# Kernel tuning notes

Hardware: AMD Instinct MI355X
Metric: run time of the kernel (lower is better)

Reference implementation:

```python
import jax, jax.numpy as jnp
import numpy as np

D_MODEL = 1024
NUM_HEADS = 16
HEAD_DIM = D_MODEL // NUM_HEADS
ROPE_THETA = 10000.0


def apply_rope(x, positions):
    # x: (B, H, S, Dh), positions: (S,) int
    half = x.shape[-1] // 2
    inv_freq = ROPE_THETA ** (-jnp.arange(half, dtype=jnp.float32) * 2.0 / x.shape[-1])  # (Dh/2,)
    ang = positions.astype(jnp.float32)[:, None] * inv_freq[None, :]  # (S, Dh/2)
    cos, sin = jnp.cos(ang), jnp.sin(ang)
    x1 = x[..., 0::2]  # (B,H,S,Dh/2)
    x2 = x[..., 1::2]
    r1 = x1 * cos - x2 * sin
    r2 = x1 * sin + x2 * cos
    return jnp.stack([r1, r2], axis=-1).reshape(x.shape)


def setup_inputs() -> dict:
    key = jax.random.key(0)
    ks = jax.random.split(key, 5)
    B, S = 2, 2048
    scale = 1.0 / np.sqrt(D_MODEL)
    x = jax.random.normal(ks[0], (B, S, D_MODEL), dtype=jnp.float32)
    Wq = jax.random.normal(ks[1], (D_MODEL, D_MODEL), dtype=jnp.float32) * scale
    Wk = jax.random.normal(ks[2], (D_MODEL, D_MODEL), dtype=jnp.float32) * scale
    Wv = jax.random.normal(ks[3], (D_MODEL, D_MODEL), dtype=jnp.float32) * scale
    Wo = jax.random.normal(ks[4], (D_MODEL, D_MODEL), dtype=jnp.float32) * scale
    token_positions = jnp.arange(S, dtype=jnp.int32)
    return {"x": x, "token_positions": token_positions, "Wq": Wq, "Wk": Wk, "Wv": Wv, "Wo": Wo}


def reference(x, token_positions, Wq, Wk, Wv, Wo):
    B, S, _ = x.shape
    # Linear is bias-free: y = x @ W.T (W: [out, in])
    def proj(W):
        y = jnp.einsum('bsd,ed->bse', x, W)
        return y.reshape(B, S, NUM_HEADS, HEAD_DIM).transpose(0, 2, 1, 3)  # (B,H,S,Dh)
    q, k, v = proj(Wq), proj(Wk), proj(Wv)
    q = apply_rope(q, token_positions)
    k = apply_rope(k, token_positions)
    scores = jnp.einsum('bhqd,bhkd->bhqk', q, k) / jnp.sqrt(jnp.float32(HEAD_DIM))
    causal = jnp.tril(jnp.ones((S, S), dtype=bool))
    scores = jnp.where(causal, scores, -jnp.inf)
    attn = jax.nn.softmax(scores, axis=-1)
    out = jnp.einsum('bhqk,bhkd->bhqd', attn, v)  # (B,H,S,Dh)
    out = out.transpose(0, 2, 1, 3).reshape(B, S, D_MODEL)
    return jnp.einsum('bsd,ed->bse', out, Wo)
```

## Files before the change

kernel.cpp:

```cpp
#include <hip/hip_runtime.h>


typedef unsigned short u16;
typedef unsigned int   u32;
typedef unsigned long long u64;
using s16x8 = __attribute__((ext_vector_type(8))) short;
using f32x4 = __attribute__((ext_vector_type(4))) float;

__device__ __forceinline__ u16 f2bf(float f) {
  union { float f; u32 u; } v; v.f = f;
  return (u16)((v.u + 0x7fffu + ((v.u >> 16) & 1u)) >> 16);
}
__device__ __forceinline__ float bf2f(u16 h) {
  union { u32 u; float f; } v; v.u = ((u32)h) << 16;
  return v.f;
}

__device__ __forceinline__ void gl2lds(const u16* g, u16* l) {
  __builtin_amdgcn_global_load_lds(
      (const __attribute__((address_space(1))) void*)g,
      (__attribute__((address_space(3))) void*)l, 16, 0, 0);
}

__global__ __launch_bounds__(256) void cvt_all(
    const float* __restrict__ x,
    const float* __restrict__ wq, const float* __restrict__ wk,
    const float* __restrict__ wv, const float* __restrict__ wo,
    u16* __restrict__ xb, u16* __restrict__ wqb, u16* __restrict__ wkb,
    u16* __restrict__ wvb, u16* __restrict__ wob) {
  int e = (blockIdx.x * 256 + threadIdx.x) * 4;
  const float* src; u16* dst; int off;
  const int XN = 4 << 20;
  if (e < XN) { src = x; dst = xb; off = e; }
  else {
    int t = e - XN; int sel = t >> 20; off = t & ((1 << 20) - 1);
    src = sel == 0 ? wq : sel == 1 ? wk : sel == 2 ? wv : wo;
    dst = sel == 0 ? wqb : sel == 1 ? wkb : sel == 2 ? wvb : wob;
  }
  float4 v = *(const float4*)(src + off);
  ushort4 o;
  o.x = f2bf(v.x); o.y = f2bf(v.y); o.z = f2bf(v.z); o.w = f2bf(v.w);
  *(ushort4*)(dst + off) = o;
}

__device__ __forceinline__ void gemm_core(
    const u16* __restrict__ A, const u16* __restrict__ W,
    u16* As, u16* Bs, int bm0, int bn0, f32x4 (&acc)[4][4]) {
  const int K = 1024;
  int tid = threadIdx.x;
  int wid = tid >> 6, lane = tid & 63, quad = lane >> 4, l15 = lane & 15;
  int wm = (wid >> 1) * 64, wn = (wid & 1) * 64;
  int ch0 = wid * 128 + lane, ch1 = ch0 + 64;
  int r0 = ch0 >> 2, c0 = (ch0 & 3) * 8;
  int r1 = ch1 >> 2, c1 = (ch1 & 3) * 8;
  const u16* Ab = A + (size_t)bm0 * K;
  const u16* Wb = W + (size_t)bn0 * K;
  u16* lA0 = As + wid * 1024; u16* lA1 = lA0 + 512;
  u16* lB0 = Bs + wid * 1024; u16* lB1 = lB0 + 512;
  for (int k0 = 0; k0 < K; k0 += 32) {
    __syncthreads();
    gl2lds(Ab + (size_t)r0 * K + k0 + c0, lA0);
    gl2lds(Ab + (size_t)r1 * K + k0 + c1, lA1);
    gl2lds(Wb + (size_t)r0 * K + k0 + c0, lB0);
    gl2lds(Wb + (size_t)r1 * K + k0 + c1, lB1);
    __syncthreads();
    s16x8 af[4], bf[4];
#pragma unroll
    for (int mi = 0; mi < 4; mi++)
      af[mi] = *(const s16x8*)(As + (wm + mi * 16 + l15) * 32 + quad * 8);
#pragma unroll
    for (int ni = 0; ni < 4; ni++)
      bf[ni] = *(const s16x8*)(Bs + (wn + ni * 16 + l15) * 32 + quad * 8);
#pragma unroll
    for (int mi = 0; mi < 4; mi++)
#pragma unroll
      for (int ni = 0; ni < 4; ni++)
        acc[mi][ni] = __builtin_amdgcn_mfma_f32_16x16x32_bf16(
            af[mi], bf[ni], acc[mi][ni], 0, 0, 0);
  }
}

__global__ __launch_bounds__(256) void gemm_qkv(
    const u16* __restrict__ xb,
    const u16* __restrict__ wq, const u16* __restrict__ wk,
    const u16* __restrict__ wv,
    u16* __restrict__ qh, u16* __restrict__ kh, u16* __restrict__ vt) {
  __shared__ __align__(16) u16 As[128 * 32];
  __shared__ __align__(16) u16 Bs[128 * 32];
  int z = blockIdx.z;
  const u16* W = (z == 0) ? wq : (z == 1) ? wk : wv;
  int bm0 = blockIdx.y * 128, bn0 = blockIdx.x * 128;
  f32x4 acc[4][4];
  const f32x4 fz = {0.f, 0.f, 0.f, 0.f};
#pragma unroll
  for (int mi = 0; mi < 4; mi++)
#pragma unroll
    for (int ni = 0; ni < 4; ni++) acc[mi][ni] = fz;
  gemm_core(xb, W, As, Bs, bm0, bn0, acc);
  int tid = threadIdx.x, wid = tid >> 6, lane = tid & 63;
  int quad = lane >> 4, l15 = lane & 15;
  int wm = (wid >> 1) * 64, wn = (wid & 1) * 64;
  if (z < 2) {
    u16* dst = (z == 0) ? qh : kh;
#pragma unroll
    for (int mi = 0; mi < 4; mi++)
#pragma unroll
      for (int ni = 0; ni < 4; ni++)
#pragma unroll
        for (int r = 0; r < 4; r++) {
          int row = bm0 + wm + mi * 16 + quad * 4 + r;
          int col = bn0 + wn + ni * 16 + l15;
          int b = row >> 11, s = row & 2047, h = col >> 6, d = col & 63;
          dst[(((size_t)(b * 16 + h)) * 2048 + s) * 64 + d] =
              f2bf(acc[mi][ni][r]);
        }
  } else {
#pragma unroll
    for (int mi = 0; mi < 4; mi++)
#pragma unroll
      for (int ni = 0; ni < 4; ni++) {
        int row0 = bm0 + wm + mi * 16 + quad * 4;
        int col = bn0 + wn + ni * 16 + l15;
        int b = row0 >> 11, s0 = row0 & 2047, h = col >> 6, d = col & 63;
        u64 pk = (u64)f2bf(acc[mi][ni][0]) |
                 ((u64)f2bf(acc[mi][ni][1]) << 16) |
                 ((u64)f2bf(acc[mi][ni][2]) << 32) |
                 ((u64)f2bf(acc[mi][ni][3]) << 48);
        *(u64*)(vt + (((size_t)(b * 16 + h)) * 64 + d) * 2048 + s0) = pk;
      }
  }
}

__global__ __launch_bounds__(256) void gemm_out(
    const u16* __restrict__ ao, const u16* __restrict__ wo,
    float* __restrict__ out) {
  __shared__ __align__(16) u16 As[128 * 32];
  __shared__ __align__(16) u16 Bs[128 * 32];
  int bm0 = blockIdx.y * 128, bn0 = blockIdx.x * 128;
  f32x4 acc[4][4];
  const f32x4 fz = {0.f, 0.f, 0.f, 0.f};
#pragma unroll
  for (int mi = 0; mi < 4; mi++)
#pragma unroll
    for (int ni = 0; ni < 4; ni++) acc[mi][ni] = fz;
  gemm_core(ao, wo, As, Bs, bm0, bn0, acc);
  int tid = threadIdx.x, wid = tid >> 6, lane = tid & 63;
  int quad = lane >> 4, l15 = lane & 15;
  int wm = (wid >> 1) * 64, wn = (wid & 1) * 64;
#pragma unroll
  for (int mi = 0; mi < 4; mi++)
#pragma unroll
    for (int ni = 0; ni < 4; ni++)
#pragma unroll
      for (int r = 0; r < 4; r++) {
        int row = bm0 + wm + mi * 16 + quad * 4 + r;
        int col = bn0 + wn + ni * 16 + l15;
        out[(size_t)row * 1024 + col] = acc[mi][ni][r];
      }
}

__global__ __launch_bounds__(256) void rope_k(
    u16* __restrict__ qh, u16* __restrict__ kh, const int* __restrict__ pos) {
  int i = blockIdx.x * 256 + threadIdx.x;
  int pair = i & 31;
  int s = (i >> 5) & 2047;
  int hb = i >> 16;
  float p = (float)pos[s];
  float freq = __expf(-0.28782313662425572f * (float)pair);
  float ang = p * freq, sn, cs;
  sincosf(ang, &sn, &cs);
  size_t base = ((size_t)hb * 2048 + s) * 64 + 2 * pair;
  {
    u32 u = *(const u32*)(qh + base);
    float x1 = bf2f((u16)(u & 0xffff)), x2 = bf2f((u16)(u >> 16));
    float r1 = (x1 * cs - x2 * sn) * 0.125f;
    float r2 = (x1 * sn + x2 * cs) * 0.125f;
    *(u32*)(qh + base) = (u32)f2bf(r1) | ((u32)f2bf(r2) << 16);
  }
  {
    u32 u = *(const u32*)(kh + base);
    float x1 = bf2f((u16)(u & 0xffff)), x2 = bf2f((u16)(u >> 16));
    float r1 = x1 * cs - x2 * sn;
    float r2 = x1 * sn + x2 * cs;
    *(u32*)(kh + base) = (u32)f2bf(r1) | ((u32)f2bf(r2) << 16);
  }
}

#define KTS 72
#define VTS 72
#define PTS 40
#define OTS 72

__global__ __launch_bounds__(256, 4) void attn_k(
    const u16* __restrict__ qh, const u16* __restrict__ kh,
    const u16* __restrict__ vt, u16* __restrict__ ao) {
  __shared__ __align__(16) u16 ks[64 * KTS];
  __shared__ __align__(16) u16 vs[64 * VTS];
  __shared__ __align__(16) u16 pt[4 * 16 * PTS];
  int bid = blockIdx.x;
  int bh = bid & 31, pi = bid >> 5;
  int b = bh >> 4, h = bh & 15;
  int tid = threadIdx.x, wid = tid >> 6, lane = tid & 63;
  int quad = lane >> 4, l15 = lane & 15;
  int qsub = wid & 1, thalf = wid >> 1;
  const u16* qbase = qh + (size_t)bh * 2048 * 64;
  const u16* kbase = kh + (size_t)bh * 2048 * 64;
  const u16* vbase = vt + (size_t)bh * 64 * 2048;
  u16* ptw = pt + wid * 16 * PTS;
  const f32x4 fz = {0.f, 0.f, 0.f, 0.f};
  int srow = tid >> 2, sc = (tid & 3) * 8;

#pragma unroll
  for (int phase = 0; phase < 2; phase++) {
    int qt = phase ? (63 - pi) : pi;
    int q0 = qt * 32, q0w = q0 + qsub * 16;
    s16x8 qf0 = *(const s16x8*)(qbase + (size_t)(q0w + l15) * 64 + quad * 8);
    s16x8 qf1 = *(const s16x8*)(qbase + (size_t)(q0w + l15) * 64 + 32 + quad * 8);
    f32x4 acc[4];
#pragma unroll
    for (int md = 0; md < 4; md++) acc[md] = fz;
    float lsum = 0.f;
    int qg = q0w + l15;
    int nt = (qt >> 1) + 1;
    uint4 rk0 = *(const uint4*)(kbase + (size_t)srow * 64 + sc);
    uint4 rk1 = *(const uint4*)(kbase + (size_t)srow * 64 + sc + 32);
    uint4 rv0 = *(const uint4*)(vbase + (size_t)srow * 2048 + sc);
    uint4 rv1 = *(const uint4*)(vbase + (size_t)srow * 2048 + sc + 32);
    for (int it = 0; it < nt; it++) {
      __syncthreads();
      *(uint4*)(ks + srow * KTS + sc) = rk0;
      *(uint4*)(ks + srow * KTS + sc + 32) = rk1;
      *(uint4*)(vs + srow * VTS + sc) = rv0;
      *(uint4*)(vs + srow * VTS + sc + 32) = rv1;
      if (it + 1 < nt) {
        int t1 = (it + 1) << 6;
        rk0 = *(const uint4*)(kbase + (size_t)(t1 + srow) * 64 + sc);
        rk1 = *(const uint4*)(kbase + (size_t)(t1 + srow) * 64 + sc + 32);
        rv0 = *(const uint4*)(vbase + (size_t)srow * 2048 + t1 + sc);
        rv1 = *(const uint4*)(vbase + (size_t)srow * 2048 + t1 + sc + 32);
      }
      __syncthreads();
      int t0 = it << 6, tb = thalf * 32;
      bool diag = (it == nt - 1);
#pragma unroll
      for (int mt = 0; mt < 2; mt++) {
        int krow = tb + mt * 16 + l15;
        s16x8 ka0 = *(const s16x8*)(ks + krow * KTS + quad * 8);
        s16x8 ka1 = *(const s16x8*)(ks + krow * KTS + 32 + quad * 8);
        f32x4 st = __builtin_amdgcn_mfma_f32_16x16x32_bf16(ka0, qf0, fz, 0, 0, 0);
        st = __builtin_amdgcn_mfma_f32_16x16x32_bf16(ka1, qf1, st, 0, 0, 0);
        u64 pk = 0;
#pragma unroll
        for (int r = 0; r < 4; r++) {
          float p = __expf(st[r]);
          if (diag) {
            int tg = t0 + tb + mt * 16 + quad * 4 + r;
            if (tg > qg) p = 0.f;
          }
          lsum += p;
          pk |= ((u64)f2bf(p)) << (16 * r);
        }
        *(u64*)(ptw + l15 * PTS + mt * 16 + quad * 4) = pk;
      }
      s16x8 pb = *(const s16x8*)(ptw + l15 * PTS + quad * 8);
#pragma unroll
      for (int md = 0; md < 4; md++) {
        s16x8 va = *(const s16x8*)(vs + (md * 16 + l15) * VTS + tb + quad * 8);
        acc[md] = __builtin_amdgcn_mfma_f32_16x16x32_bf16(va, pb, acc[md], 0, 0, 0);
      }
    }
    lsum += __shfl_xor(lsum, 16, 64);
    lsum += __shfl_xor(lsum, 32, 64);
    __syncthreads();
    float* redo = (float*)ks;
    float* redl = (float*)vs;
    if (thalf == 1) {
#pragma unroll
      for (int md = 0; md < 4; md++)
#pragma unroll
        for (int r = 0; r < 4; r++)
          redo[(qsub * 64 + lane) * 16 + md * 4 + r] = acc[md][r];
      redl[qsub * 64 + lane] = lsum;
    }
    __syncthreads();
    if (thalf == 0) {
#pragma unroll
      for (int md = 0; md < 4; md++)
#pragma unroll
        for (int r = 0; r < 4; r++)
          acc[md][r] += redo[(qsub * 64 + lane) * 16 + md * 4 + r];
      lsum += redl[qsub * 64 + lane];
      float rl = 1.0f / lsum;
      u16* ow = pt + qsub * 16 * OTS;
#pragma unroll
      for (int md = 0; md < 4; md++) {
        u64 ok = 0;
#pragma unroll
        for (int r = 0; r < 4; r++)
          ok |= ((u64)f2bf(acc[md][r] * rl)) << (16 * r);
        *(u64*)(ow + l15 * OTS + md * 16 + quad * 4) = ok;
      }
      int qq = lane >> 2, dc = lane & 3;
      uint4 o0 = *(uint4*)(ow + qq * OTS + dc * 16);
      uint4 o1 = *(uint4*)(ow + qq * OTS + dc * 16 + 8);
      size_t orow = (size_t)b * 2048 + q0 + qsub * 16 + qq;
      *(uint4*)(ao + orow * 1024 + h * 64 + dc * 16) = o0;
      *(uint4*)(ao + orow * 1024 + h * 64 + dc * 16 + 8) = o1;
    }
  }
}

extern "C" void kernel_launch(void* const* d_in, const int* in_sizes, int n_in,
                              void* d_out, int out_size, void* d_ws,
                              size_t ws_size, hipStream_t stream) {
  const float* x  = (const float*)d_in[0];
  const int* pos  = (const int*)d_in[1];
  const float* Wq = (const float*)d_in[2];
  const float* Wk = (const float*)d_in[3];
  const float* Wv = (const float*)d_in[4];
  const float* Wo = (const float*)d_in[5];
  float* out = (float*)d_out;

  char* ws = (char*)d_ws;
  const size_t MB = 1u << 20;
  u16* xb  = (u16*)(ws);
  u16* wqb = (u16*)(ws + 8 * MB);
  u16* wkb = (u16*)(ws + 10 * MB);
  u16* wvb = (u16*)(ws + 12 * MB);
  u16* wob = (u16*)(ws + 14 * MB);
  u16* qhb = (u16*)(ws + 16 * MB);
  u16* khb = (u16*)(ws + 24 * MB);
  u16* vtb = (u16*)(ws + 32 * MB);
  u16* ao  = xb;

  cvt_all<<<8192, 256, 0, stream>>>(x, Wq, Wk, Wv, Wo,
                                    xb, wqb, wkb, wvb, wob);
  gemm_qkv<<<dim3(8, 32, 3), 256, 0, stream>>>(xb, wqb, wkb, wvb,
                                               qhb, khb, vtb);
  rope_k<<<8192, 256, 0, stream>>>(qhb, khb, pos);
  attn_k<<<1024, 256, 0, stream>>>(qhb, khb, vtb, ao);
  gemm_out<<<dim3(8, 32), 256, 0, stream>>>(ao, wob, out);
}
```

Measured before the change: 214.8 us.

## Fuse RoPE into QKV GEMM epilogue and load K/V fragments directly in attention

Applies rotary embedding (and the softmax scale folded with log2e) inside the QKV GEMM epilogue using a lane shuffle to fetch the pair partner, eliminating the separate rope kernel and its extra read/write of Q and K. The attention kernel stops staging K/V tiles in LDS and instead loads MFMA fragments directly from global memory with register prefetch, removing per-tile barriers; exp is switched to exp2. The trade-off is less coalesced global loads and more sincos work per GEMM output element.

Measured after the change: 493.0 us. +129.5%, slower.

```diff
diff --git a/kernel.cpp b/kernel.cpp
--- a/kernel.cpp
+++ b/kernel.cpp
@@ -10,10 +10,6 @@
 __device__ __forceinline__ u16 f2bf(float f) {
   union { float f; u32 u; } v; v.f = f;
   return (u16)((v.u + 0x7fffu + ((v.u >> 16) & 1u)) >> 16);
-}
-__device__ __forceinline__ float bf2f(u16 h) {
-  union { u32 u; float f; } v; v.u = ((u32)h) << 16;
-  return v.f;
 }
 
 __device__ __forceinline__ void gl2lds(const u16* g, u16* l) {
@@ -83,7 +79,7 @@
 __global__ __launch_bounds__(256) void gemm_qkv(
     const u16* __restrict__ xb,
     const u16* __restrict__ wq, const u16* __restrict__ wk,
-    const u16* __restrict__ wv,
+    const u16* __restrict__ wv, const int* __restrict__ pos,
     u16* __restrict__ qh, u16* __restrict__ kh, u16* __restrict__ vt) {
   __shared__ __align__(16) u16 As[128 * 32];
   __shared__ __align__(16) u16 Bs[128 * 32];
@@ -102,18 +98,33 @@
   int wm = (wid >> 1) * 64, wn = (wid & 1) * 64;
   if (z < 2) {
     u16* dst = (z == 0) ? qh : kh;
+    float sc = (z == 0) ? 0.18033688011112042f : 1.0f;
+    float frq[4], sgn[4];
+#pragma unroll
+    for (int ni = 0; ni < 4; ni++) {
+      int d = (bn0 + wn + ni * 16 + l15) & 63;
+      frq[ni] = __expf(-0.28782313662425572f * (float)(d >> 1));
+      sgn[ni] = (d & 1) ? 1.f : -1.f;
+    }
 #pragma unroll
     for (int mi = 0; mi < 4; mi++)
 #pragma unroll
-      for (int ni = 0; ni < 4; ni++)
-#pragma unroll
-        for (int r = 0; r < 4; r++) {
-          int row = bm0 + wm + mi * 16 + quad * 4 + r;
+      for (int r = 0; r < 4; r++) {
+        int row = bm0 + wm + mi * 16 + quad * 4 + r;
+        int b = row >> 11, s = row & 2047;
+        float pv = (float)pos[s];
+#pragma unroll
+        for (int ni = 0; ni < 4; ni++) {
+          float v = acc[mi][ni][r];
+          float prt = __shfl_xor(v, 1, 64);
+          float ang = pv * frq[ni], sn, cs;
+          sincosf(ang, &sn, &cs);
+          float res = (v * cs + sgn[ni] * prt * sn) * sc;
           int col = bn0 + wn + ni * 16 + l15;
-          int b = row >> 11, s = row & 2047, h = col >> 6, d = col & 63;
-          dst[(((size_t)(b * 16 + h)) * 2048 + s) * 64 + d] =
-              f2bf(acc[mi][ni][r]);
+          int h = col >> 6, d = col & 63;
+          dst[(((size_t)(b * 16 + h)) * 2048 + s) * 64 + d] = f2bf(res);
         }
+      }
   } else {
 #pragma unroll
     for (int mi = 0; mi < 4; mi++)
@@ -159,44 +170,15 @@
       }
 }
 
-__global__ __launch_bounds__(256) void rope_k(
-    u16* __restrict__ qh, u16* __restrict__ kh, const int* __restrict__ pos) {
-  int i = blockIdx.x * 256 + threadIdx.x;
-  int pair = i & 31;
-  int s = (i >> 5) & 2047;
-  int hb = i >> 16;
-  float p = (float)pos[s];
-  float freq = __expf(-0.28782313662425572f * (float)pair);
-  float ang = p * freq, sn, cs;
-  sincosf(ang, &sn, &cs);
-  size_t base = ((size_t)hb * 2048 + s) * 64 + 2 * pair;
-  {
-    u32 u = *(const u32*)(qh + base);
-    float x1 = bf2f((u16)(u & 0xffff)), x2 = bf2f((u16)(u >> 16));
-    float r1 = (x1 * cs - x2 * sn) * 0.125f;
-    float r2 = (x1 * sn + x2 * cs) * 0.125f;
-    *(u32*)(qh + base) = (u32)f2bf(r1) | ((u32)f2bf(r2) << 16);
-  }
-  {
-    u32 u = *(const u32*)(kh + base);
-    float x1 = bf2f((u16)(u & 0xffff)), x2 = bf2f((u16)(u >> 16));
-    float r1 = x1 * cs - x2 * sn;
-    float r2 = x1 * sn + x2 * cs;
-    *(u32*)(kh + base) = (u32)f2bf(r1) | ((u32)f2bf(r2) << 16);
-  }
-}
-
-#define KTS 72
-#define VTS 72
 #define PTS 40
 #define OTS 72
 
 __global__ __launch_bounds__(256, 4) void attn_k(
     const u16* __restrict__ qh, const u16* __restrict__ kh,
     const u16* __restrict__ vt, u16* __restrict__ ao) {
-  __shared__ __align__(16) u16 ks[64 * KTS];
-  __shared__ __align__(16) u16 vs[64 * VTS];
   __shared__ __align__(16) u16 pt[4 * 16 * PTS];
+  __shared__ float redo[128 * 17];
+  __shared__ float redl[128];
   int bid = blockIdx.x;
   int bh = bid & 31, pi = bid >> 5;
   int b = bh >> 4, h = bh & 15;
@@ -208,10 +190,11 @@
   const u16* vbase = vt + (size_t)bh * 64 * 2048;
   u16* ptw = pt + wid * 16 * PTS;
   const f32x4 fz = {0.f, 0.f, 0.f, 0.f};
-  int srow = tid >> 2, sc = (tid & 3) * 8;
+  int tb = thalf * 32;
 
 #pragma unroll
   for (int phase = 0; phase < 2; phase++) {
+    __syncthreads();
     int qt = phase ? (63 - pi) : pi;
     int q0 = qt * 32, q0w = q0 + qsub * 16;
     s16x8 qf0 = *(const s16x8*)(qbase + (size_t)(q0w + l15) * 64 + quad * 8);
@@ -222,37 +205,38 @@
     float lsum = 0.f;
     int qg = q0w + l15;
     int nt = (qt >> 1) + 1;
-    uint4 rk0 = *(const uint4*)(kbase + (size_t)srow * 64 + sc);
-    uint4 rk1 = *(const uint4*)(kbase + (size_t)srow * 64 + sc + 32);
-    uint4 rv0 = *(const uint4*)(vbase + (size_t)srow * 2048 + sc);
-    uint4 rv1 = *(const uint4*)(vbase + (size_t)srow * 2048 + sc + 32);
+    s16x8 ka[4];
+    {
+      const u16* kr = kbase + (size_t)(tb + l15) * 64 + quad * 8;
+      ka[0] = *(const s16x8*)(kr);
+      ka[1] = *(const s16x8*)(kr + 32);
+      ka[2] = *(const s16x8*)(kr + 1024);
+      ka[3] = *(const s16x8*)(kr + 1024 + 32);
+    }
     for (int it = 0; it < nt; it++) {
-      __syncthreads();
-      *(uint4*)(ks + srow * KTS + sc) = rk0;
-      *(uint4*)(ks + srow * KTS + sc + 32) = rk1;
-      *(uint4*)(vs + srow * VTS + sc) = rv0;
-      *(uint4*)(vs + srow * VTS + sc + 32) = rv1;
+      int t0 = it << 6;
+      s16x8 va[4];
+#pragma unroll
+      for (int md = 0; md < 4; md++)
+        va[md] = *(const s16x8*)(vbase + (size_t)(md * 16 + l15) * 2048 +
+                                 t0 + tb + quad * 8);
+      s16x8 kn[4];
       if (it + 1 < nt) {
-        int t1 = (it + 1) << 6;
-        rk0 = *(const uint4*)(kbase + (size_t)(t1 + srow) * 64 + sc);
-        rk1 = *(const uint4*)(kbase + (size_t)(t1 + srow) * 64 + sc + 32);
-        rv0 = *(const uint4*)(vbase + (size_t)srow * 2048 + t1 + sc);
-        rv1 = *(const uint4*)(vbase + (size_t)srow * 2048 + t1 + sc + 32);
-      }
-      __syncthreads();
-      int t0 = it << 6, tb = thalf * 32;
+        const u16* kr = kbase + (size_t)(t0 + 64 + tb + l15) * 64 + quad * 8;
+        kn[0] = *(const s16x8*)(kr);
+        kn[1] = *(const s16x8*)(kr + 32);
+        kn[2] = *(const s16x8*)(kr + 1024);
+        kn[3] = *(const s16x8*)(kr + 1024 + 32);
+      }
       bool diag = (it == nt - 1);
 #pragma unroll
       for (int mt = 0; mt < 2; mt++) {
-        int krow = tb + mt * 16 + l15;
-        s16x8 ka0 = *(const s16x8*)(ks + krow * KTS + quad * 8);
-        s16x8 ka1 = *(const s16x8*)(ks + krow * KTS + 32 + quad * 8);
-        f32x4 st = __builtin_amdgcn_mfma_f32_16x16x32_bf16(ka0, qf0, fz, 0, 0, 0);
-        st = __builtin_amdgcn_mfma_f32_16x16x32_bf16(ka1, qf1, st, 0, 0, 0);
+        f32x4 st = __builtin_amdgcn_mfma_f32_16x16x32_bf16(ka[2 * mt], qf0, fz, 0, 0, 0);
+        st = __builtin_amdgcn_mfma_f32_16x16x32_bf16(ka[2 * mt + 1], qf1, st, 0, 0, 0);
         u64 pk = 0;
 #pragma unroll
         for (int r = 0; r < 4; r++) {
-          float p = __expf(st[r]);
+          float p = __builtin_amdgcn_exp2f(st[r]);
           if (diag) {
             int tg = t0 + tb + mt * 16 + quad * 4 + r;
             if (tg > qg) p = 0.f;
@@ -264,22 +248,19 @@
       }
       s16x8 pb = *(const s16x8*)(ptw + l15 * PTS + quad * 8);
 #pragma unroll
-      for (int md = 0; md < 4; md++) {
-        s16x8 va = *(const s16x8*)(vs + (md * 16 + l15) * VTS + tb + quad * 8);
-        acc[md] = __builtin_amdgcn_mfma_f32_16x16x32_bf16(va, pb, acc[md], 0, 0, 0);
-      }
+      for (int md = 0; md < 4; md++)
+        acc[md] = __builtin_amdgcn_mfma_f32_16x16x32_bf16(va[md], pb, acc[md], 0, 0, 0);
+#pragma unroll
+      for (int j = 0; j < 4; j++) ka[j] = kn[j];
     }
     lsum += __shfl_xor(lsum, 16, 64);
     lsum += __shfl_xor(lsum, 32, 64);
-    __syncthreads();
-    float* redo = (float*)ks;
-    float* redl = (float*)vs;
     if (thalf == 1) {
 #pragma unroll
       for (int md = 0; md < 4; md++)
 #pragma unroll
         for (int r = 0; r < 4; r++)
-          redo[(qsub * 64 + lane) * 16 + md * 4 + r] = acc[md][r];
+          redo[(qsub * 64 + lane) * 17 + md * 4 + r] = acc[md][r];
       redl[qsub * 64 + lane] = lsum;
     }
     __syncthreads();
@@ -288,7 +269,7 @@
       for (int md = 0; md < 4; md++)
 #pragma unroll
         for (int r = 0; r < 4; r++)
-          acc[md][r] += redo[(qsub * 64 + lane) * 16 + md * 4 + r];
+          acc[md][r] += redo[(qsub * 64 + lane) * 17 + md * 4 + r];
       lsum += redl[qsub * 64 + lane];
       float rl = 1.0f / lsum;
       u16* ow = pt + qsub * 16 * OTS;
@@ -335,9 +316,8 @@
 
   cvt_all<<<8192, 256, 0, stream>>>(x, Wq, Wk, Wv, Wo,
                                     xb, wqb, wkb, wvb, wob);
-  gemm_qkv<<<dim3(8, 32, 3), 256, 0, stream>>>(xb, wqb, wkb, wvb,
+  gemm_qkv<<<dim3(8, 32, 3), 256, 0, stream>>>(xb, wqb, wkb, wvb, pos,
                                                qhb, khb, vtb);
-  rope_k<<<8192, 256, 0, stream>>>(qhb, khb, pos);
   attn_k<<<1024, 256, 0, stream>>>(qhb, khb, vtb, ao);
   gemm_out<<<dim3(8, 32), 256, 0, stream>>>(ao, wob, out);
 }
```
